# Performance work log

Hardware: AMD Instinct MI355X
Metric: run time of the kernel (lower is better)

The kernel has to match this reference:

```python
import jax, jax.numpy as jnp
import numpy as np

GAMMA = 0.3          # surrogate gradient scale (LinearSpikeMC.gamma)
K = 2                # num_channels: multi-compartment count
T = 3                # timesteps
B = 4                # batch
LABELS = 10
CONV_CFG = [64, 64, 128, 128, 256, 256, 256, 512, 512, 512, 512, 512, 512]
POOL_AFTER = {1, 3, 6, 9}  # avg-pool after these conv indices (VGG16 'A' positions)


@jax.custom_vjp
def spike_mc(even, odd):
    # one-hot multi-compartment spike: fire where even>0 AND odd>=0
    return jnp.where((even > 0.0) & (odd >= 0.0), 1.0, 0.0).astype(even.dtype)

def _spike_fwd(even, odd):
    return spike_mc(even, odd), (even, odd)

def _spike_bwd(res, g):
    even, odd = res
    ge = GAMMA * jnp.maximum(1.0 - jnp.abs(even), 0.0) * g
    go = -GAMMA * jnp.maximum(1.0 - jnp.abs(odd), 0.0) * g
    # torch backward loop never writes the last odd compartment's grad
    go = go.at[-1].set(0.0)
    return ge, go

spike_mc.defvjp(_spike_fwd, _spike_bwd)


def conv3x3(x, w):
    return jax.lax.conv_general_dilated(
        x, w, (1, 1), 'SAME', dimension_numbers=('NCHW', 'OIHW', 'NCHW'))


def avgpool2(x):
    b, c, h, w = x.shape
    return x.reshape(b, c, h // 2, 2, w // 2, 2).mean(axis=(3, 5))


def lif(mem, syn, thr, leak):
    # leaky integrate; compartment i fires when 2^i*thr < mem <= 2^{i+1}*thr
    mem = leak * mem + syn
    pw = (2.0 ** jnp.arange(K, dtype=mem.dtype)).reshape((K,) + (1,) * mem.ndim)
    even = mem[None] / (pw * thr) - 1.0
    odd = 1.0 - mem[None] / (2.0 * pw * thr)
    sp = spike_mc(even, odd)            # [K, ...] one-hot spikes
    val = jnp.sum(pw * sp, axis=0)      # decoded value sum_i 2^i * s_i
    mem = mem - thr * val               # soft reset (reset_to_zero=0)
    return mem, val


def setup_inputs():
    key = jax.random.key(0)
    ks = jax.random.split(key, 32)
    inp = {"x": jax.random.normal(ks[0], (B, 3, 32, 32), jnp.float32)}
    in_c = 3
    for i, out_c in enumerate(CONV_CFG):
        std = float(np.sqrt(2.0 / (9.0 * out_c)))  # kaiming init from _initialize_weights2
        inp[f"w{i}"] = jax.random.normal(ks[1 + i], (out_c, in_c, 3, 3), jnp.float32) * std
        in_c = out_c
    inp["fc0"] = jax.random.normal(ks[20], (4096, 512 * 2 * 2), jnp.float32) * 0.01
    inp["fc1"] = jax.random.normal(ks[21], (4096, 4096), jnp.float32) * 0.01
    inp["fc2"] = jax.random.normal(ks[22], (LABELS, 4096), jnp.float32) * 0.01
    inp["thr"] = jnp.ones((15,), jnp.float32)   # per-layer thresholds
    inp["leak"] = jnp.ones((15,), jnp.float32)  # per-layer leaks
    return inp


def reference(x, w0, w1, w2, w3, w4, w5, w6, w7, w8, w9, w10, w11, w12,
              fc0, fc1, fc2, thr, leak):
    conv_ws = [w0, w1, w2, w3, w4, w5, w6, w7, w8, w9, w10, w11, w12]
    b = x.shape[0]
    # membranes sized at each conv's output resolution (neuron_init)
    mems = []
    s = 32
    for i, c in enumerate(CONV_CFG):
        mems.append(jnp.zeros((b, c, s, s), x.dtype))
        if i in POOL_AFTER:
            s //= 2
    carry0 = (tuple(mems),
              jnp.zeros((b, 4096), x.dtype),
              jnp.zeros((b, 4096), x.dtype),
              jnp.zeros((b, fc2.shape[0]), x.dtype))

    def step(carry, _):
        mems_c, m0, m1, logits = carry
        out = x  # analog input each timestep (input_encoding=1)
        new = []
        for i in range(13):
            m, out = lif(mems_c[i], conv3x3(out, conv_ws[i]), thr[i], leak[i])
            new.append(m)
            if i in POOL_AFTER:
                out = avgpool2(out)
        out = out.reshape(b, -1)
        m0, out = lif(m0, out @ fc0.T, thr[13], leak[13])
        m1, out = lif(m1, out @ fc1.T, thr[14], leak[14])
        logits = logits + out @ fc2.T  # final linear accumulates, no spiking
        return (tuple(new), m0, m1, logits), None

    carry, _ = jax.lax.scan(step, carry0, None, length=T)
    return carry[3]
```

## Files before the change

kernel.cpp:

```cpp
#include <hip/hip_runtime.h>


#define BATCH 4

__device__ __forceinline__ float lif_update(float mem_in, float syn, float thr,
                                            float leak, float* mem_out) {
    float m = leak * mem_in + syn;
    float val = 0.f;
    if ((m / thr - 1.f > 0.f) && (1.f - m / (2.f * thr) >= 0.f)) val += 1.f;
    if ((m / (2.f * thr) - 1.f > 0.f) && (1.f - m / (4.f * thr) >= 0.f)) val += 2.f;
    *mem_out = m - thr * val;
    return val;
}

__global__ void conv_lif0_kernel(const float* __restrict__ in,
                                 const float* __restrict__ w,
                                 float* __restrict__ out0,
                                 float* __restrict__ out1,
                                 float* __restrict__ out2,
                                 const float* __restrict__ thr_v,
                                 const float* __restrict__ leak_v,
                                 int IC, int OC, int H, int W, int n) {
    int idx = blockIdx.x * blockDim.x + threadIdx.x;
    if (idx >= n) return;
    int x  = idx % W;
    int y  = (idx / W) % H;
    int oc = (idx / (W * H)) % OC;
    int b  = idx / (W * H * OC);

    const float* wp = w + (size_t)oc * IC * 9;
    const float* ip = in + (size_t)b * IC * H * W;

    float syn = 0.f;
    for (int ic = 0; ic < IC; ++ic) {
        const float* ipc = ip + (size_t)ic * H * W;
        const float* wpc = wp + ic * 9;
#pragma unroll
        for (int ky = 0; ky < 3; ++ky) {
            int yy = y + ky - 1;
            if (yy < 0 || yy >= H) continue;
#pragma unroll
            for (int kx = 0; kx < 3; ++kx) {
                int xx = x + kx - 1;
                if (xx < 0 || xx >= W) continue;
                syn = fmaf(ipc[yy * W + xx], wpc[ky * 3 + kx], syn);
            }
        }
    }
    float thr = thr_v[0], leak = leak_v[0];
    float m = 0.f;
    float v0 = lif_update(m, syn, thr, leak, &m);
    float v1 = lif_update(m, syn, thr, leak, &m);
    float v2 = lif_update(m, syn, thr, leak, &m);
    out0[idx] = v0;
    out1[idx] = v1;
    out2[idx] = v2;
}

__device__ __forceinline__ void mid_load3(float v[3][9],
                                          const float* __restrict__ p0,
                                          const float* __restrict__ p1,
                                          const float* __restrict__ p2,
                                          const int off[9], const bool msk[9]) {
#pragma unroll
    for (int k = 0; k < 9; ++k) {
        v[0][k] = msk[k] ? p0[off[k]] : 0.f;
        v[1][k] = msk[k] ? p1[off[k]] : 0.f;
        v[2][k] = msk[k] ? p2[off[k]] : 0.f;
    }
}

template <int OCT, int ICT>
__device__ __forceinline__ void mid_fma3(const float v[3][9],
                                         const float* __restrict__ wlds,
                                         int ic, float acc[3][OCT]) {
#pragma unroll
    for (int q = 0; q < OCT; ++q) {
        const float* wq = wlds + ((size_t)q * ICT + ic) * 9;
        float wr[9];
#pragma unroll
        for (int k = 0; k < 9; ++k) wr[k] = wq[k];
#pragma unroll
        for (int k = 0; k < 9; ++k) {
            acc[0][q] = fmaf(v[0][k], wr[k], acc[0][q]);
            acc[1][q] = fmaf(v[1][k], wr[k], acc[1][q]);
            acc[2][q] = fmaf(v[2][k], wr[k], acc[2][q]);
        }
    }
}

template <int OCT, int NW, int POOL, int ICT, int W_>
__global__ __launch_bounds__(NW * 64)
void conv_mid3_kernel(const float* __restrict__ in0,
                      const float* __restrict__ in1,
                      const float* __restrict__ in2,
                      const float* __restrict__ w,
                      float* __restrict__ out0,
                      float* __restrict__ out1,
                      float* __restrict__ out2,
                      const float* __restrict__ thr_v,
                      const float* __restrict__ leak_v,
                      int layer, int OC) {
    constexpr int HW = W_ * W_;
    constexpr int CHUNKS = HW / 64;
    constexpr int RPW = 64 / W_;
    constexpr int ICPW = ICT / NW;
    static_assert((ICPW & 1) == 0, "icpw must be even");

    int tid = threadIdx.x;
    int lane = tid & 63;
    int wv = tid >> 6;
    int ocg = OC / OCT;
    int bid = blockIdx.x;
    int g  = bid % ocg;
    int ch = (bid / ocg) % CHUNKS;
    int b  = bid / (ocg * CHUNKS);
    int y = ch * RPW + lane / W_;
    int x = lane % W_;
    int oc0 = g * OCT;

    int off[9];
    bool msk[9];
#pragma unroll
    for (int ky = 0; ky < 3; ++ky)
#pragma unroll
        for (int kx = 0; kx < 3; ++kx) {
            int yy = y + ky - 1, xx = x + kx - 1;
            bool v = (yy >= 0 && yy < W_ && xx >= 0 && xx < W_);
            msk[ky * 3 + kx] = v;
            off[ky * 3 + kx] = v ? yy * W_ + xx : 0;
        }

    size_t boff = (size_t)b * ICT * HW;
    const float* i0 = in0 + boff;
    const float* i1 = in1 + boff;
    const float* i2 = in2 + boff;
    float* const outs[3] = {out0, out1, out2};

    __shared__ float wlds[OCT * ICT * 9];
    {
        const float* wsrc = w + (size_t)oc0 * ICT * 9;
        for (int s = tid; s < OCT * ICT * 9; s += NW * 64) wlds[s] = wsrc[s];
    }
    __syncthreads();

    float acc[3][OCT];
#pragma unroll
    for (int t = 0; t < 3; ++t)
#pragma unroll
        for (int q = 0; q < OCT; ++q) acc[t][q] = 0.f;

    int ic0 = wv * ICPW;
    int icend = ic0 + ICPW;

    float va[3][9], vb[3][9];
    mid_load3(va, i0 + (size_t)ic0 * HW, i1 + (size_t)ic0 * HW,
              i2 + (size_t)ic0 * HW, off, msk);

    for (int ic = ic0; ic < icend; ic += 2) {
        mid_load3(vb, i0 + (size_t)(ic + 1) * HW, i1 + (size_t)(ic + 1) * HW,
                  i2 + (size_t)(ic + 1) * HW, off, msk);
        mid_fma3<OCT, ICT>(va, wlds, ic, acc);
        int icn = (ic + 2 < icend) ? ic + 2 : ic;
        mid_load3(va, i0 + (size_t)icn * HW, i1 + (size_t)icn * HW,
                  i2 + (size_t)icn * HW, off, msk);
        mid_fma3<OCT, ICT>(vb, wlds, ic + 1, acc);
    }

    __shared__ float red[NW][OCT][64];
    __shared__ float vals[OCT][64];
    float thr = thr_v[layer], leak = leak_v[layer];
    float mem_reg = 0.f;
    int eq = tid >> 6, ep = tid & 63;
    constexpr int Wo = W_ / 2, Ho = W_ / 2;

#pragma unroll
    for (int t = 0; t < 3; ++t) {
        __syncthreads();
#pragma unroll
        for (int q = 0; q < OCT; ++q) red[wv][q][lane] = acc[t][q];
        __syncthreads();
        if (tid < OCT * 64) {
            float sum = 0.f;
#pragma unroll
            for (int q = 0; q < NW; ++q) sum += red[q][eq][ep];
            float val = lif_update(mem_reg, sum, thr, leak, &mem_reg);
            if (POOL) {
                vals[eq][ep] = val;
            } else {
                size_t idx = (size_t)(b * OC + oc0 + eq) * HW + ch * 64 + ep;
                outs[t][idx] = val;
            }
        }
        if (POOL) {
            __syncthreads();
            if (tid < OCT * 16) {
                int q = tid >> 4, s = tid & 15;
                int pr = s / Wo, pc = s % Wo;
                float pv = 0.25f * (vals[q][(2 * pr) * W_ + 2 * pc] +
                                    vals[q][(2 * pr) * W_ + 2 * pc + 1] +
                                    vals[q][(2 * pr + 1) * W_ + 2 * pc] +
                                    vals[q][(2 * pr + 1) * W_ + 2 * pc + 1]);
                size_t pidx = ((size_t)(b * OC + oc0 + q) * Ho +
                               (ch * (RPW >> 1) + pr)) * Wo + pc;
                outs[t][pidx] = pv;
            }
        }
    }
}

template <int S, int NW, int POOL>
__global__ __launch_bounds__(NW * 64)
void conv_small4_3_kernel(const float* __restrict__ in0,
                          const float* __restrict__ in1,
                          const float* __restrict__ in2,
                          const float* __restrict__ w,
                          float* __restrict__ out0,
                          float* __restrict__ out1,
                          float* __restrict__ out2,
                          const float* __restrict__ thr_v,
                          const float* __restrict__ leak_v,
                          int layer, int IC, int OC) {
    constexpr int SS = S * S;
    constexpr int M = 4 * SS;
    constexpr int LOG2M = (S == 4) ? 6 : 4;
    int tid = threadIdx.x;
    int lane = tid & 63;
    int wv = tid >> 6;
    int oc = blockIdx.x;

    const float* const ins[3] = {in0, in1, in2};
    float* const outs[3] = {out0, out1, out2};
    const float* wrow = w + (size_t)oc * IC * 9;

    __shared__ float red[NW][M];
    __shared__ float pvs[M];
    float thr = thr_v[layer], leak = leak_v[layer];
    float mem_reg = 0.f;

#pragma unroll
    for (int t = 0; t < 3; ++t) {
        const float* inb = ins[t];
        float acc[M];
#pragma unroll
        for (int i = 0; i < M; ++i) acc[i] = 0.f;

        for (int ic = lane + (wv << 6); ic < IC; ic += NW * 64) {
            const float* wp = wrow + (size_t)ic * 9;
            float wvv[9];
#pragma unroll
            for (int k = 0; k < 9; ++k) wvv[k] = wp[k];
#pragma unroll
            for (int b = 0; b < 4; ++b) {
                const float4* ip = (const float4*)(inb + (size_t)(b * IC + ic) * SS);
                float pv[SS];
#pragma unroll
                for (int q = 0; q < SS / 4; ++q) {
                    float4 t4 = ip[q];
                    pv[4 * q + 0] = t4.x;
                    pv[4 * q + 1] = t4.y;
                    pv[4 * q + 2] = t4.z;
                    pv[4 * q + 3] = t4.w;
                }
#pragma unroll
                for (int y = 0; y < S; ++y)
#pragma unroll
                    for (int x = 0; x < S; ++x) {
                        float a = acc[b * SS + y * S + x];
#pragma unroll
                        for (int ky = 0; ky < 3; ++ky) {
                            int yy = y + ky - 1;
                            if (yy < 0 || yy >= S) continue;
#pragma unroll
                            for (int kx = 0; kx < 3; ++kx) {
                                int xx = x + kx - 1;
                                if (xx < 0 || xx >= S) continue;
                                a = fmaf(pv[yy * S + xx], wvv[ky * 3 + kx], a);
                            }
                        }
                        acc[b * SS + y * S + x] = a;
                    }
            }
        }

#pragma unroll
        for (int step = 0; step < LOG2M; ++step) {
            const int offx = 1 << step;
            const int half = M >> (step + 1);
            const bool hi = (lane & offx) != 0;
#pragma unroll
            for (int i = 0; i < half; ++i) {
                float sent = hi ? acc[i] : acc[i + half];
                float got = __shfl_xor(sent, offx);
                acc[i] = (hi ? acc[i + half] : acc[i]) + got;
            }
        }
        float sum = acc[0];
#pragma unroll
        for (int offx = M; offx < 64; offx <<= 1) sum += __shfl_xor(sum, offx);

        __syncthreads();
        int o = (int)(__brev((unsigned)(lane & (M - 1))) >> (32 - LOG2M));
        if (lane < M) red[wv][o] = sum;
        __syncthreads();

        if (tid < M) {
            float tot = 0.f;
#pragma unroll
            for (int q = 0; q < NW; ++q) tot += red[q][tid];
            int b = tid / SS, p = tid % SS;
            float val = lif_update(mem_reg, tot, thr, leak, &mem_reg);
            if (POOL) {
                pvs[tid] = val;
            } else {
                size_t idx = (size_t)(b * OC + oc) * SS + p;
                outs[t][idx] = val;
            }
        }
        if (POOL) {
            __syncthreads();
            constexpr int Sh = S / 2, SSh = Sh * Sh;
            if (tid < 4 * SSh) {
                int b = tid / SSh, q = tid % SSh;
                int pr = q / Sh, pc = q % Sh;
                float pv = 0.25f * (pvs[b * SS + (2 * pr) * S + 2 * pc] +
                                    pvs[b * SS + (2 * pr) * S + 2 * pc + 1] +
                                    pvs[b * SS + (2 * pr + 1) * S + 2 * pc] +
                                    pvs[b * SS + (2 * pr + 1) * S + 2 * pc + 1]);
                outs[t][((size_t)(b * OC + oc) * Sh + pr) * Sh + pc] = pv;
            }
        }
    }
}

__global__ void fc_lif3_kernel(const float* __restrict__ in0,
                               const float* __restrict__ in1,
                               const float* __restrict__ in2,
                               const float* __restrict__ w,
                               float* __restrict__ out0,
                               float* __restrict__ out1,
                               float* __restrict__ out2,
                               const float* __restrict__ thr_v,
                               const float* __restrict__ leak_v,
                               int layer, int Kd, int N) {
    int wave = (blockIdx.x * blockDim.x + threadIdx.x) >> 6;
    int lane = threadIdx.x & 63;
    if (wave >= N) return;
    int j = wave;
    int K4 = Kd >> 2;
    const float4* wp = (const float4*)(w + (size_t)j * Kd);
    const float4* ip[3] = {(const float4*)in0, (const float4*)in1, (const float4*)in2};
    float* const outs[3] = {out0, out1, out2};

    float a[3][4];
#pragma unroll
    for (int t = 0; t < 3; ++t)
#pragma unroll
        for (int b = 0; b < 4; ++b) a[t][b] = 0.f;

    for (int k = lane; k < K4; k += 64) {
        float4 wv = wp[k];
#pragma unroll
        for (int t = 0; t < 3; ++t)
#pragma unroll
            for (int b = 0; b < 4; ++b) {
                float4 v = ip[t][b * K4 + k];
                a[t][b] = fmaf(wv.x, v.x, fmaf(wv.y, v.y,
                          fmaf(wv.z, v.z, fmaf(wv.w, v.w, a[t][b]))));
            }
    }
#pragma unroll
    for (int t = 0; t < 3; ++t)
#pragma unroll
        for (int b = 0; b < 4; ++b)
#pragma unroll
            for (int off = 32; off > 0; off >>= 1)
                a[t][b] += __shfl_xor(a[t][b], off);

    if (lane == 0) {
        float thr = thr_v[layer], leak = leak_v[layer];
#pragma unroll
        for (int b = 0; b < BATCH; ++b) {
            float m = 0.f;
#pragma unroll
            for (int t = 0; t < 3; ++t) {
                float val = lif_update(m, a[t][b], thr, leak, &m);
                outs[t][(size_t)b * N + j] = val;
            }
        }
    }
}

__global__ void fc2_acc3_kernel(const float* __restrict__ in0,
                                const float* __restrict__ in1,
                                const float* __restrict__ in2,
                                const float* __restrict__ w,
                                float* __restrict__ logits,
                                int Kd, int L) {
    int o = blockIdx.x;
    int l = o % L;
    int b = o / L;
    int K4 = Kd >> 2;
    const float4* ip[3] = {(const float4*)(in0 + (size_t)b * Kd),
                           (const float4*)(in1 + (size_t)b * Kd),
                           (const float4*)(in2 + (size_t)b * Kd)};
    const float4* wp = (const float4*)(w + (size_t)l * Kd);
    float st[3] = {0.f, 0.f, 0.f};
    for (int k = threadIdx.x; k < K4; k += 64) {
        float4 wv = wp[k];
#pragma unroll
        for (int t = 0; t < 3; ++t) {
            float4 iv = ip[t][k];
            st[t] = fmaf(iv.x, wv.x, fmaf(iv.y, wv.y,
                    fmaf(iv.z, wv.z, fmaf(iv.w, wv.w, st[t]))));
        }
    }
#pragma unroll
    for (int t = 0; t < 3; ++t)
#pragma unroll
        for (int off = 32; off > 0; off >>= 1) st[t] += __shfl_xor(st[t], off);
    if (threadIdx.x == 0) logits[o] = (st[0] + st[1]) + st[2];
}

extern "C" void kernel_launch(void* const* d_in, const int* in_sizes, int n_in,
                              void* d_out, int out_size, void* d_ws, size_t ws_size,
                              hipStream_t stream) {
    const float* x = (const float*)d_in[0];
    const float* convw[13];
    for (int i = 0; i < 13; ++i) convw[i] = (const float*)d_in[1 + i];
    const float* fc0 = (const float*)d_in[14];
    const float* fc1 = (const float*)d_in[15];
    const float* fc2 = (const float*)d_in[16];
    const float* thr = (const float*)d_in[17];
    const float* leak = (const float*)d_in[18];

    static const int IC[13] = {3, 64, 64, 128, 128, 256, 256, 256, 512, 512, 512, 512, 512};
    static const int OC[13] = {64, 64, 128, 128, 256, 256, 256, 512, 512, 512, 512, 512, 512};

    float* ws = (float*)d_ws;
    float* A[3];
    float* B[3];
    size_t off = 0;
    for (int i = 0; i < 3; ++i) { A[i] = ws + off; off += 262144; }
    for (int i = 0; i < 3; ++i) { B[i] = ws + off; off += 262144; }

    {
        int n = BATCH * 64 * 32 * 32;
        conv_lif0_kernel<<<(n + 255) / 256, 256, 0, stream>>>(
            x, convw[0], A[0], A[1], A[2], thr, leak, 3, 64, 32, 32, n);
    }

    float** src = A;
    float** dst = B;

    conv_mid3_kernel<8, 8, 1, 64, 32><<<BATCH * 16 * (OC[1] / 8), 512, 0, stream>>>(
        src[0], src[1], src[2], convw[1], dst[0], dst[1], dst[2],
        thr, leak, 1, OC[1]);
    { float** tmp = src; src = dst; dst = tmp; }

    conv_mid3_kernel<4, 8, 0, 64, 16><<<BATCH * 4 * (OC[2] / 4), 512, 0, stream>>>(
        src[0], src[1], src[2], convw[2], dst[0], dst[1], dst[2],
        thr, leak, 2, OC[2]);
    { float** tmp = src; src = dst; dst = tmp; }

    conv_mid3_kernel<4, 8, 1, 128, 16><<<BATCH * 4 * (OC[3] / 4), 512, 0, stream>>>(
        src[0], src[1], src[2], convw[3], dst[0], dst[1], dst[2],
        thr, leak, 3, OC[3]);
    { float** tmp = src; src = dst; dst = tmp; }

    conv_mid3_kernel<2, 8, 0, 128, 8><<<BATCH * (OC[4] / 2), 512, 0, stream>>>(
        src[0], src[1], src[2], convw[4], dst[0], dst[1], dst[2],
        thr, leak, 4, OC[4]);
    { float** tmp = src; src = dst; dst = tmp; }

    conv_mid3_kernel<2, 8, 0, 256, 8><<<BATCH * (OC[5] / 2), 512, 0, stream>>>(
        src[0], src[1], src[2], convw[5], dst[0], dst[1], dst[2],
        thr, leak, 5, OC[5]);
    { float** tmp = src; src = dst; dst = tmp; }

    conv_mid3_kernel<2, 8, 1, 256, 8><<<BATCH * (OC[6] / 2), 512, 0, stream>>>(
        src[0], src[1], src[2], convw[6], dst[0], dst[1], dst[2],
        thr, leak, 6, OC[6]);
    { float** tmp = src; src = dst; dst = tmp; }

    for (int i = 7; i <= 12; ++i) {
        if (i == 7)
            conv_small4_3_kernel<4, 4, 0><<<OC[i], 256, 0, stream>>>(
                src[0], src[1], src[2], convw[i], dst[0], dst[1], dst[2],
                thr, leak, i, IC[i], OC[i]);
        else if (i == 8)
            conv_small4_3_kernel<4, 8, 0><<<OC[i], 512, 0, stream>>>(
                src[0], src[1], src[2], convw[i], dst[0], dst[1], dst[2],
                thr, leak, i, IC[i], OC[i]);
        else if (i == 9)
            conv_small4_3_kernel<4, 8, 1><<<OC[i], 512, 0, stream>>>(
                src[0], src[1], src[2], convw[i], dst[0], dst[1], dst[2],
                thr, leak, i, IC[i], OC[i]);
        else
            conv_small4_3_kernel<2, 8, 0><<<OC[i], 512, 0, stream>>>(
                src[0], src[1], src[2], convw[i], dst[0], dst[1], dst[2],
                thr, leak, i, IC[i], OC[i]);
        float** tmp = src; src = dst; dst = tmp;
    }

    fc_lif3_kernel<<<(4096 * 64) / 256, 256, 0, stream>>>(
        src[0], src[1], src[2], fc0, dst[0], dst[1], dst[2],
        thr, leak, 13, 2048, 4096);
    { float** tmp = src; src = dst; dst = tmp; }

    fc_lif3_kernel<<<(4096 * 64) / 256, 256, 0, stream>>>(
        src[0], src[1], src[2], fc1, dst[0], dst[1], dst[2],
        thr, leak, 14, 4096, 4096);
    { float** tmp = src; src = dst; dst = tmp; }

    fc2_acc3_kernel<<<BATCH * 10, 64, 0, stream>>>(
        src[0], src[1], src[2], fc2, (float*)d_out, 4096, 10);
}
```

Before: 692.2 us.

## Store spike activations as zero-padded float4 time-interleaved tensors for conv layers 0-6

```diff
diff --git a/kernel.cpp b/kernel.cpp
--- a/kernel.cpp
+++ b/kernel.cpp
@@ -13,14 +13,14 @@
     return val;
 }
 
-__global__ void conv_lif0_kernel(const float* __restrict__ in,
-                                 const float* __restrict__ w,
-                                 float* __restrict__ out0,
-                                 float* __restrict__ out1,
-                                 float* __restrict__ out2,
-                                 const float* __restrict__ thr_v,
-                                 const float* __restrict__ leak_v,
-                                 int IC, int OC, int H, int W, int n) {
+__global__ void conv_lif0_pad_kernel(const float* __restrict__ in,
+                                     const float* __restrict__ w,
+                                     float4* __restrict__ out4,
+                                     const float* __restrict__ thr_v,
+                                     const float* __restrict__ leak_v,
+                                     int n) {
+    constexpr int H = 32, W = 32, IC = 3, OC = 64;
+    constexpr int PW = 34, PP = 34 * 34;
     int idx = blockIdx.x * blockDim.x + threadIdx.x;
     if (idx >= n) return;
     int x  = idx % W;
@@ -52,57 +52,62 @@
     float v0 = lif_update(m, syn, thr, leak, &m);
     float v1 = lif_update(m, syn, thr, leak, &m);
     float v2 = lif_update(m, syn, thr, leak, &m);
-    out0[idx] = v0;
-    out1[idx] = v1;
-    out2[idx] = v2;
-}
-
-__device__ __forceinline__ void mid_load3(float v[3][9],
-                                          const float* __restrict__ p0,
-                                          const float* __restrict__ p1,
-                                          const float* __restrict__ p2,
-                                          const int off[9], const bool msk[9]) {
-#pragma unroll
-    for (int k = 0; k < 9; ++k) {
-        v[0][k] = msk[k] ? p0[off[k]] : 0.f;
-        v[1][k] = msk[k] ? p1[off[k]] : 0.f;
-        v[2][k] = msk[k] ? p2[off[k]] : 0.f;
-    }
+    size_t cell = (size_t)(b * OC + oc) * PP + (size_t)(y + 1) * PW + (x + 1);
+    out4[cell] = make_float4(v0, v1, v2, 0.f);
+
+    if (idx < 256 * 132) {
+        int bc = idx / 132;
+        int c  = idx % 132;
+        int row, col;
+        if (c < 34) { row = 0; col = c; }
+        else if (c < 68) { row = 33; col = c - 34; }
+        else { int d = c - 68; row = 1 + (d >> 1); col = (d & 1) * 33; }
+        out4[(size_t)bc * PP + (size_t)row * PW + col] = make_float4(0.f, 0.f, 0.f, 0.f);
+    }
+}
+
+template <int PW>
+__device__ __forceinline__ void pad_load9(float4 tv[9],
+                                          const float4* __restrict__ lp) {
+#pragma unroll
+    for (int ky = 0; ky < 3; ++ky)
+#pragma unroll
+        for (int kx = 0; kx < 3; ++kx) tv[ky * 3 + kx] = lp[ky * PW + kx];
 }
 
 template <int OCT, int ICT>
-__device__ __forceinline__ void mid_fma3(const float v[3][9],
-                                         const float* __restrict__ wlds,
-                                         int ic, float acc[3][OCT]) {
+__device__ __forceinline__ void pad_fma3(const float4 tv[9],
+                                         const float* __restrict__ wp,
+                                         float acc[3][OCT]) {
 #pragma unroll
     for (int q = 0; q < OCT; ++q) {
-        const float* wq = wlds + ((size_t)q * ICT + ic) * 9;
+        const float* wq = wp + (size_t)q * ICT * 9;
         float wr[9];
 #pragma unroll
         for (int k = 0; k < 9; ++k) wr[k] = wq[k];
 #pragma unroll
         for (int k = 0; k < 9; ++k) {
-            acc[0][q] = fmaf(v[0][k], wr[k], acc[0][q]);
-            acc[1][q] = fmaf(v[1][k], wr[k], acc[1][q]);
-            acc[2][q] = fmaf(v[2][k], wr[k], acc[2][q]);
-        }
-    }
-}
-
-template <int OCT, int NW, int POOL, int ICT, int W_>
+            acc[0][q] = fmaf(tv[k].x, wr[k], acc[0][q]);
+            acc[1][q] = fmaf(tv[k].y, wr[k], acc[1][q]);
+            acc[2][q] = fmaf(tv[k].z, wr[k], acc[2][q]);
+        }
+    }
+}
+
+template <int OCT, int NW, int POOL, int PLAIN, int ICT, int W_>
 __global__ __launch_bounds__(NW * 64)
-void conv_mid3_kernel(const float* __restrict__ in0,
-                      const float* __restrict__ in1,
-                      const float* __restrict__ in2,
+void conv_pad3_kernel(const float4* __restrict__ in4,
                       const float* __restrict__ w,
+                      float4* __restrict__ out4,
                       float* __restrict__ out0,
                       float* __restrict__ out1,
                       float* __restrict__ out2,
                       const float* __restrict__ thr_v,
                       const float* __restrict__ leak_v,
                       int layer, int OC) {
-    constexpr int HW = W_ * W_;
-    constexpr int CHUNKS = HW / 64;
+    constexpr int PW = W_ + 2;
+    constexpr int PP = PW * PW;
+    constexpr int CHUNKS = (W_ * W_) / 64;
     constexpr int RPW = 64 / W_;
     constexpr int ICPW = ICT / NW;
     static_assert((ICPW & 1) == 0, "icpw must be even");
@@ -119,30 +124,9 @@
     int x = lane % W_;
     int oc0 = g * OCT;
 
-    int off[9];
-    bool msk[9];
-#pragma unroll
-    for (int ky = 0; ky < 3; ++ky)
-#pragma unroll
-        for (int kx = 0; kx < 3; ++kx) {
-            int yy = y + ky - 1, xx = x + kx - 1;
-            bool v = (yy >= 0 && yy < W_ && xx >= 0 && xx < W_);
-            msk[ky * 3 + kx] = v;
-            off[ky * 3 + kx] = v ? yy * W_ + xx : 0;
-        }
-
-    size_t boff = (size_t)b * ICT * HW;
-    const float* i0 = in0 + boff;
-    const float* i1 = in1 + boff;
-    const float* i2 = in2 + boff;
-    float* const outs[3] = {out0, out1, out2};
-
-    __shared__ float wlds[OCT * ICT * 9];
-    {
-        const float* wsrc = w + (size_t)oc0 * ICT * 9;
-        for (int s = tid; s < OCT * ICT * 9; s += NW * 64) wlds[s] = wsrc[s];
-    }
-    __syncthreads();
+    const float4* lp = in4 + ((size_t)b * ICT + (size_t)wv * ICPW) * PP
+                       + (size_t)y * PW + x;
+    const float* wbase = w + ((size_t)oc0 * ICT + (size_t)wv * ICPW) * 9;
 
     float acc[3][OCT];
 #pragma unroll
@@ -150,29 +134,23 @@
 #pragma unroll
         for (int q = 0; q < OCT; ++q) acc[t][q] = 0.f;
 
-    int ic0 = wv * ICPW;
-    int icend = ic0 + ICPW;
-
-    float va[3][9], vb[3][9];
-    mid_load3(va, i0 + (size_t)ic0 * HW, i1 + (size_t)ic0 * HW,
-              i2 + (size_t)ic0 * HW, off, msk);
-
-    for (int ic = ic0; ic < icend; ic += 2) {
-        mid_load3(vb, i0 + (size_t)(ic + 1) * HW, i1 + (size_t)(ic + 1) * HW,
-                  i2 + (size_t)(ic + 1) * HW, off, msk);
-        mid_fma3<OCT, ICT>(va, wlds, ic, acc);
-        int icn = (ic + 2 < icend) ? ic + 2 : ic;
-        mid_load3(va, i0 + (size_t)icn * HW, i1 + (size_t)icn * HW,
-                  i2 + (size_t)icn * HW, off, msk);
-        mid_fma3<OCT, ICT>(vb, wlds, ic + 1, acc);
+    float4 tva[9], tvb[9];
+    pad_load9<PW>(tva, lp);
+
+    for (int i = 0; i < ICPW; i += 2) {
+        pad_load9<PW>(tvb, lp + PP);
+        pad_fma3<OCT, ICT>(tva, wbase + (size_t)i * 9, acc);
+        const float4* lpn = (i + 2 < ICPW) ? lp + 2 * PP : lp;
+        pad_load9<PW>(tva, lpn);
+        pad_fma3<OCT, ICT>(tvb, wbase + (size_t)(i + 1) * 9, acc);
+        lp += 2 * PP;
     }
 
     __shared__ float red[NW][OCT][64];
-    __shared__ float vals[OCT][64];
     float thr = thr_v[layer], leak = leak_v[layer];
     float mem_reg = 0.f;
     int eq = tid >> 6, ep = tid & 63;
-    constexpr int Wo = W_ / 2, Ho = W_ / 2;
+    float4 myv = make_float4(0.f, 0.f, 0.f, 0.f);
 
 #pragma unroll
     for (int t = 0; t < 3; ++t) {
@@ -185,26 +163,64 @@
 #pragma unroll
             for (int q = 0; q < NW; ++q) sum += red[q][eq][ep];
             float val = lif_update(mem_reg, sum, thr, leak, &mem_reg);
-            if (POOL) {
-                vals[eq][ep] = val;
+            if (t == 0) myv.x = val;
+            else if (t == 1) myv.y = val;
+            else myv.z = val;
+        }
+    }
+
+    if (!POOL) {
+        if (tid < OCT * 64) {
+            int yo = ch * RPW + ep / W_;
+            int xo = ep % W_;
+            size_t cell = (size_t)(b * OC + oc0 + eq) * PP
+                          + (size_t)(yo + 1) * PW + (xo + 1);
+            out4[cell] = myv;
+        }
+    } else {
+        __shared__ float4 vals4[OCT][64];
+        if (tid < OCT * 64) vals4[eq][ep] = myv;
+        __syncthreads();
+        constexpr int Wo = W_ / 2;
+        if (tid < OCT * 16) {
+            int q = tid >> 4, s = tid & 15;
+            int pr = s / Wo, pc = s % Wo;
+            float4 a = vals4[q][(2 * pr) * W_ + 2 * pc];
+            float4 bb = vals4[q][(2 * pr) * W_ + 2 * pc + 1];
+            float4 c = vals4[q][(2 * pr + 1) * W_ + 2 * pc];
+            float4 d = vals4[q][(2 * pr + 1) * W_ + 2 * pc + 1];
+            float4 pv;
+            pv.x = 0.25f * (a.x + bb.x + c.x + d.x);
+            pv.y = 0.25f * (a.y + bb.y + c.y + d.y);
+            pv.z = 0.25f * (a.z + bb.z + c.z + d.z);
+            pv.w = 0.f;
+            int prg = ch * (RPW >> 1) + pr;
+            if (PLAIN) {
+                size_t pidx = ((size_t)(b * OC + oc0 + q) * Wo + prg) * Wo + pc;
+                out0[pidx] = pv.x;
+                out1[pidx] = pv.y;
+                out2[pidx] = pv.z;
             } else {
-                size_t idx = (size_t)(b * OC + oc0 + eq) * HW + ch * 64 + ep;
-                outs[t][idx] = val;
-            }
-        }
-        if (POOL) {
-            __syncthreads();
-            if (tid < OCT * 16) {
-                int q = tid >> 4, s = tid & 15;
-                int pr = s / Wo, pc = s % Wo;
-                float pv = 0.25f * (vals[q][(2 * pr) * W_ + 2 * pc] +
-                                    vals[q][(2 * pr) * W_ + 2 * pc + 1] +
-                                    vals[q][(2 * pr + 1) * W_ + 2 * pc] +
-                                    vals[q][(2 * pr + 1) * W_ + 2 * pc + 1]);
-                size_t pidx = ((size_t)(b * OC + oc0 + q) * Ho +
-                               (ch * (RPW >> 1) + pr)) * Wo + pc;
-                outs[t][pidx] = pv;
-            }
+                constexpr int PWo = Wo + 2, PPo = PWo * PWo;
+                size_t cell = (size_t)(b * OC + oc0 + q) * PPo
+                              + (size_t)(prg + 1) * PWo + (pc + 1);
+                out4[cell] = pv;
+            }
+        }
+    }
+
+    if (!PLAIN && ch == 0) {
+        constexpr int S = POOL ? W_ / 2 : W_;
+        constexpr int PWo = S + 2, PPo = PWo * PWo;
+        constexpr int NH = 4 * S + 4;
+        for (int s2 = tid; s2 < OCT * NH; s2 += NW * 64) {
+            int q = s2 / NH, c = s2 % NH;
+            int row, col;
+            if (c < S + 2) { row = 0; col = c; }
+            else if (c < 2 * (S + 2)) { row = S + 1; col = c - (S + 2); }
+            else { int d2 = c - 2 * (S + 2); row = 1 + (d2 >> 1); col = (d2 & 1) * (S + 1); }
+            out4[(size_t)(b * OC + oc0 + q) * PPo + (size_t)row * PWo + col] =
+                make_float4(0.f, 0.f, 0.f, 0.f);
         }
     }
 }
@@ -437,51 +453,41 @@
     static const int IC[13] = {3, 64, 64, 128, 128, 256, 256, 256, 512, 512, 512, 512, 512};
     static const int OC[13] = {64, 64, 128, 128, 256, 256, 256, 512, 512, 512, 512, 512, 512};
 
-    float* ws = (float*)d_ws;
+    float* wsf = (float*)d_ws;
+    float4* P0 = (float4*)wsf;
+    float4* P1 = P0 + 300000;
+    float* base = wsf + (size_t)2 * 300000 * 4;
     float* A[3];
     float* B[3];
-    size_t off = 0;
-    for (int i = 0; i < 3; ++i) { A[i] = ws + off; off += 262144; }
-    for (int i = 0; i < 3; ++i) { B[i] = ws + off; off += 262144; }
+    for (int i = 0; i < 3; ++i) { A[i] = base + (size_t)i * 65536; }
+    for (int i = 0; i < 3; ++i) { B[i] = base + (size_t)(3 + i) * 65536; }
 
     {
         int n = BATCH * 64 * 32 * 32;
-        conv_lif0_kernel<<<(n + 255) / 256, 256, 0, stream>>>(
-            x, convw[0], A[0], A[1], A[2], thr, leak, 3, 64, 32, 32, n);
-    }
+        conv_lif0_pad_kernel<<<(n + 255) / 256, 256, 0, stream>>>(
+            x, convw[0], P0, thr, leak, n);
+    }
+
+    conv_pad3_kernel<4, 8, 1, 0, 64, 32><<<BATCH * 16 * (OC[1] / 4), 512, 0, stream>>>(
+        P0, convw[1], P1, nullptr, nullptr, nullptr, thr, leak, 1, OC[1]);
+
+    conv_pad3_kernel<4, 8, 0, 0, 64, 16><<<BATCH * 4 * (OC[2] / 4), 512, 0, stream>>>(
+        P1, convw[2], P0, nullptr, nullptr, nullptr, thr, leak, 2, OC[2]);
+
+    conv_pad3_kernel<4, 8, 1, 0, 128, 16><<<BATCH * 4 * (OC[3] / 4), 512, 0, stream>>>(
+        P0, convw[3], P1, nullptr, nullptr, nullptr, thr, leak, 3, OC[3]);
+
+    conv_pad3_kernel<2, 8, 0, 0, 128, 8><<<BATCH * (OC[4] / 2), 512, 0, stream>>>(
+        P1, convw[4], P0, nullptr, nullptr, nullptr, thr, leak, 4, OC[4]);
+
+    conv_pad3_kernel<2, 8, 0, 0, 256, 8><<<BATCH * (OC[5] / 2), 512, 0, stream>>>(
+        P0, convw[5], P1, nullptr, nullptr, nullptr, thr, leak, 5, OC[5]);
+
+    conv_pad3_kernel<2, 8, 1, 1, 256, 8><<<BATCH * (OC[6] / 2), 512, 0, stream>>>(
+        P1, convw[6], P0 , A[0], A[1], A[2], thr, leak, 6, OC[6]);
 
     float** src = A;
     float** dst = B;
-
-    conv_mid3_kernel<8, 8, 1, 64, 32><<<BATCH * 16 * (OC[1] / 8), 512, 0, stream>>>(
-        src[0], src[1], src[2], convw[1], dst[0], dst[1], dst[2],
-        thr, leak, 1, OC[1]);
-    { float** tmp = src; src = dst; dst = tmp; }
-
-    conv_mid3_kernel<4, 8, 0, 64, 16><<<BATCH * 4 * (OC[2] / 4), 512, 0, stream>>>(
-        src[0], src[1], src[2], convw[2], dst[0], dst[1], dst[2],
-        thr, leak, 2, OC[2]);
-    { float** tmp = src; src = dst; dst = tmp; }
-
-    conv_mid3_kernel<4, 8, 1, 128, 16><<<BATCH * 4 * (OC[3] / 4), 512, 0, stream>>>(
-        src[0], src[1], src[2], convw[3], dst[0], dst[1], dst[2],
-        thr, leak, 3, OC[3]);
-    { float** tmp = src; src = dst; dst = tmp; }
-
-    conv_mid3_kernel<2, 8, 0, 128, 8><<<BATCH * (OC[4] / 2), 512, 0, stream>>>(
-        src[0], src[1], src[2], convw[4], dst[0], dst[1], dst[2],
-        thr, leak, 4, OC[4]);
-    { float** tmp = src; src = dst; dst = tmp; }
-
-    conv_mid3_kernel<2, 8, 0, 256, 8><<<BATCH * (OC[5] / 2), 512, 0, stream>>>(
-        src[0], src[1], src[2], convw[5], dst[0], dst[1], dst[2],
-        thr, leak, 5, OC[5]);
-    { float** tmp = src; src = dst; dst = tmp; }
-
-    conv_mid3_kernel<2, 8, 1, 256, 8><<<BATCH * (OC[6] / 2), 512, 0, stream>>>(
-        src[0], src[1], src[2], convw[6], dst[0], dst[1], dst[2],
-        thr, leak, 6, OC[6]);
-    { float** tmp = src; src = dst; dst = tmp; }
 
     for (int i = 7; i <= 12; ++i) {
         if (i == 7)
```

New measurement: 641.4 us. 1.08x faster.
